# Performance work log

Hardware: AMD Instinct MI355X
Metric: run time of the kernel (lower is better)

The kernel has to match this reference:

```python
import jax, jax.numpy as jnp
import numpy as np

BS, P, D, D_WM, H, W = 64, 512, 1024, 1024, 16, 128
HD = D_WM // H
SCALE = 1.0 / np.sqrt(HD)


def setup_inputs() -> dict:
    key = jax.random.key(0)
    ks = jax.random.split(key, 10)
    s = 0.02
    x_all = jax.random.normal(ks[0], (BS, P, D), dtype=jnp.float32)
    reset_mask_all = jax.random.randint(ks[1], (BS, P), 0, 50) == 0
    return {
        'x_all': x_all,
        'reset_mask_all': reset_mask_all,
        'Wq_w': jax.random.normal(ks[2], (D, D_WM), dtype=jnp.float32) * s,
        'Wq_b': jnp.zeros((D_WM,), jnp.float32),
        'Wk_w': jax.random.normal(ks[3], (D, D_WM), dtype=jnp.float32) * s,
        'Wk_b': jnp.zeros((D_WM,), jnp.float32),
        'Wv_w': jax.random.normal(ks[4], (D, D_WM), dtype=jnp.float32) * s,
        'Wv_b': jnp.zeros((D_WM,), jnp.float32),
        'Wo_w': jax.random.normal(ks[5], (D_WM, D), dtype=jnp.float32) * s,
        'Wo_b': jnp.zeros((D,), jnp.float32),
    }


def _forward_span(x_all, reset_mask_all, Wq_w, Wq_b, Wk_w, Wk_b, Wv_w, Wv_b, Wo_w, Wo_b):
    # Batched projections over all P tokens (matches forward_span)
    q_all = jnp.einsum('bpd,de->bpe', x_all, Wq_w) + Wq_b
    k_all = jnp.einsum('bpd,de->bpe', x_all, Wk_w) + Wk_b
    v_all = jnp.einsum('bpd,de->bpe', x_all, Wv_w) + Wv_b

    def step(carry, inp):
        K, V, valid, ptr = carry  # [BS,W,D_WM], [BS,W,D_WM], [BS,W] bool, [BS] int
        q, k, v, reset_t = inp    # [BS,D_WM] x3, [BS] bool
        # doc-boundary reset
        valid = valid & ~reset_t[:, None]
        ptr = jnp.where(reset_t, 0, ptr)
        # ring-buffer write at ptr (one-hot broadcast, as in the original)
        wm = jnp.arange(W)[None, :] == ptr[:, None]          # [BS,W] bool
        wf = wm.astype(K.dtype)[:, :, None]                   # [BS,W,1]
        K = K * (1.0 - wf) + k[:, None, :] * wf
        V = V * (1.0 - wf) + v[:, None, :] * wf
        valid = valid | wm
        # windowed multi-head attention over the buffer
        qh = q.reshape(BS, H, HD)
        Kh = K.reshape(BS, W, H, HD)
        Vh = V.reshape(BS, W, H, HD)
        attn = jnp.einsum('bhd,bwhd->bhw', qh, Kh) * SCALE
        attn = jnp.where(valid[:, None, :], attn, -jnp.inf)
        attn = jax.nn.softmax(attn, axis=-1)
        attn = jnp.nan_to_num(attn)
        out = jnp.einsum('bhw,bwhd->bhd', attn, Vh).reshape(BS, D_WM)
        y = out @ Wo_w + Wo_b
        ptr = (ptr + 1) % W
        return (K, V, valid, ptr), y

    init = (
        jnp.zeros((BS, W, D_WM), x_all.dtype),
        jnp.zeros((BS, W, D_WM), x_all.dtype),
        jnp.zeros((BS, W), bool),
        jnp.zeros((BS,), jnp.int32),
    )
    xs = (
        q_all.transpose(1, 0, 2),
        k_all.transpose(1, 0, 2),
        v_all.transpose(1, 0, 2),
        reset_mask_all.T,
    )
    _, ys = jax.lax.scan(step, init, xs)  # ys: [P,BS,D]
    return ys.transpose(1, 0, 2)


def reference(x_all, reset_mask_all, Wq_w, Wq_b, Wk_w, Wk_b, Wv_w, Wv_b, Wo_w, Wo_b):
    return _forward_span(x_all, reset_mask_all, Wq_w, Wq_b, Wk_w, Wk_b, Wv_w, Wv_b, Wo_w, Wo_b)
```

## Files before the change

### kernel.cpp

```cpp
#include <hip/hip_runtime.h>
#include <stdint.h>

typedef __bf16 bf16_t;
typedef __bf16 bf16x8 __attribute__((ext_vector_type(8)));
typedef __bf16 bf16x4 __attribute__((ext_vector_type(4)));
typedef float  f32x4  __attribute__((ext_vector_type(4)));

constexpr int cBS = 64, cP = 512, cD = 1024, cDWM = 1024, cH = 16, cHD = 64, cW = 128;
constexpr int cVTP = 672;
constexpr int cM = cBS * cP;
constexpr float cSCALE = 0.125f;

__device__ __forceinline__ void gld_lds16(const void* g, void* l) {
#if __has_builtin(__builtin_amdgcn_global_load_lds)
  __builtin_amdgcn_global_load_lds(
      (__attribute__((address_space(1))) void*)g,
      (__attribute__((address_space(3))) void*)l, 16, 0, 0);
#else
  *(bf16x8*)l = *(const bf16x8*)g;
#endif
}

__global__ void cvt_x_k(const float* __restrict__ X, bf16_t* __restrict__ Y, int n) {
  int i = (blockIdx.x * blockDim.x + threadIdx.x) * 4;
  if (i >= n) return;
  float4 v = *(const float4*)(X + i);
  bf16x4 o;
  o[0] = (bf16_t)v.x; o[1] = (bf16_t)v.y; o[2] = (bf16_t)v.z; o[3] = (bf16_t)v.w;
  *(bf16x4*)(Y + i) = o;
}

__global__ void cvt_wt_k(const float* __restrict__ W0, const float* __restrict__ W1,
                         const float* __restrict__ W2, const float* __restrict__ W3,
                         bf16_t* __restrict__ T0, bf16_t* __restrict__ T1,
                         bf16_t* __restrict__ T2, bf16_t* __restrict__ T3) {
  __shared__ float tile[32][33];
  const float* Wsrc; bf16_t* Tdst;
  switch (blockIdx.z) {
    case 0: Wsrc = W0; Tdst = T0; break;
    case 1: Wsrc = W1; Tdst = T1; break;
    case 2: Wsrc = W2; Tdst = T2; break;
    default: Wsrc = W3; Tdst = T3; break;
  }
  const int n0 = blockIdx.x * 32, k0 = blockIdx.y * 32;
  const int c = threadIdx.x & 31, r8 = threadIdx.x >> 5;
#pragma unroll
  for (int q = 0; q < 4; ++q) {
    int row = r8 + q * 8;
    tile[row][c] = Wsrc[(size_t)(k0 + row) * 1024 + n0 + c];
  }
  __syncthreads();
#pragma unroll
  for (int q = 0; q < 4; ++q) {
    int row = r8 + q * 8;
    Tdst[(size_t)(n0 + row) * 1024 + k0 + c] = (bf16_t)tile[c][row];
  }
}

__global__ void resets2_k(const int* __restrict__ mask, int* __restrict__ r) {
  __shared__ int sm[cP];
  const int b = blockIdx.x, t = threadIdx.x;
  sm[t] = mask[b * cP + t] ? t : 0;
  __syncthreads();
#pragma unroll
  for (int d = 1; d < cP; d <<= 1) {
    int u = (t >= d) ? sm[t - d] : 0;
    __syncthreads();
    if (u > sm[t]) sm[t] = u;
    __syncthreads();
  }
  r[b * cP + t] = sm[t];
}

__global__ __launch_bounds__(512, 2)
void gemm_qkv8_k(const bf16_t* __restrict__ A, const bf16_t* __restrict__ Wt,
                 const float* __restrict__ bq, const float* __restrict__ bk,
                 const float* __restrict__ bvv,
                 bf16_t* __restrict__ Qh, bf16_t* __restrict__ Kh,
                 bf16_t* __restrict__ Vt) {
  __shared__ __align__(16) char LDS[131072];
  const int tid = threadIdx.x;
  const int wid = tid >> 6, ln = tid & 63;
  const int ln15 = ln & 15, g4 = ln >> 4;
  const int wr = wid >> 2, wc = wid & 3;

  const int g = blockIdx.x + 12 * blockIdx.y;
  const int xcd = g & 7, s = g >> 3;
  const int nb = s % 12, mloc = s / 12;
  const int m0 = (xcd * 16 + mloc) * 256, n0 = nb * 256;

  const bf16_t* Ab = A + (size_t)m0 * 1024;
  const bf16_t* Bb = Wt + (size_t)n0 * 1024;

  const int srow = (tid >> 6) * 16 + (tid & 15);
  const int kc = (tid >> 4) & 3;
  const size_t aoff = (size_t)srow * 1024 + (size_t)(kc * 8);
  char* const lbase = LDS + tid * 16;

  const int lane16 = (g4 * 16 + ln15) * 16;
  const int abase = (wr * 8) * 1024 + lane16;
  const int bbase = 32768 + (wc * 4) * 1024 + lane16;

  f32x4 acc[8][4];
#pragma unroll
  for (int i = 0; i < 8; ++i)
#pragma unroll
    for (int j = 0; j < 4; ++j) acc[i][j] = {0.f, 0.f, 0.f, 0.f};

  bf16x8 bq_[4];

#define STAGE_A(buf, kh, j) do {                                              \
    const bf16_t* gp_ = Ab + (size_t)((j) * 64 + (kh) * 32) + aoff;           \
    char* lp_ = lbase + (buf) * 65536 + (kh) * 16384;                         \
    gld_lds16(gp_, lp_);                                                      \
    gld_lds16(gp_ + (size_t)128 * 1024, lp_ + 8192);                          \
  } while (0)

#define STAGE_B(buf, kh, j) do {                                              \
    const bf16_t* gp_ = Bb + (size_t)((j) * 64 + (kh) * 32) + aoff;           \
    char* lp_ = lbase + (buf) * 65536 + (kh) * 16384 + 32768;                 \
    gld_lds16(gp_, lp_);                                                      \
    gld_lds16(gp_ + (size_t)128 * 1024, lp_ + 8192);                          \
  } while (0)

#define NOSTAGE ((void)0)
#define VM4 asm volatile("s_waitcnt vmcnt(4)" ::: "memory")
#define VM0 asm volatile("s_waitcnt vmcnt(0)" ::: "memory")
#define NOVM ((void)0)

#define PHASE_F(buf, kh, STAGE, VME) do {                                     \
    const char* Ar_ = LDS + (buf) * 65536 + (kh) * 16384 + abase;             \
    const char* Br_ = LDS + (buf) * 65536 + (kh) * 16384 + bbase;             \
    bf16x8 af_[4];                                                            \
    af_[0] = *(const bf16x8*)(Ar_);                                           \
    af_[1] = *(const bf16x8*)(Ar_ + 1024);                                    \
    af_[2] = *(const bf16x8*)(Ar_ + 2048);                                    \
    af_[3] = *(const bf16x8*)(Ar_ + 3072);                                    \
    bq_[0] = *(const bf16x8*)(Br_);                                           \
    bq_[1] = *(const bf16x8*)(Br_ + 1024);                                    \
    bq_[2] = *(const bf16x8*)(Br_ + 2048);                                    \
    bq_[3] = *(const bf16x8*)(Br_ + 3072);                                    \
    STAGE;                                                                    \
    __builtin_amdgcn_s_barrier();                                             \
    asm volatile("s_waitcnt lgkmcnt(0)" ::: "memory");                        \
    __builtin_amdgcn_s_setprio(1);                                            \
    _Pragma("unroll")                                                         \
    for (int mi_ = 0; mi_ < 4; ++mi_)                                         \
      _Pragma("unroll")                                                       \
      for (int nj_ = 0; nj_ < 4; ++nj_)                                       \
        acc[mi_][nj_] = __builtin_amdgcn_mfma_f32_16x16x32_bf16(              \
            af_[mi_], bq_[nj_], acc[mi_][nj_], 0, 0, 0);                      \
    __builtin_amdgcn_s_setprio(0);                                            \
    VME;                                                                      \
    __builtin_amdgcn_s_barrier();                                             \
  } while (0)

#define PHASE_R(buf, kh, STAGE, VME) do {                                     \
    const char* Ar_ = LDS + (buf) * 65536 + (kh) * 16384 + abase + 4096;      \
    bf16x8 af_[4];                                                            \
    af_[0] = *(const bf16x8*)(Ar_);                                           \
    af_[1] = *(const bf16x8*)(Ar_ + 1024);                                    \
    af_[2] = *(const bf16x8*)(Ar_ + 2048);                                    \
    af_[3] = *(const bf16x8*)(Ar_ + 3072);                                    \
    STAGE;                                                                    \
    __builtin_amdgcn_s_barrier();                                             \
    asm volatile("s_waitcnt lgkmcnt(0)" ::: "memory");                        \
    __builtin_amdgcn_s_setprio(1);                                            \
    _Pragma("unroll")                                                         \
    for (int mi_ = 0; mi_ < 4; ++mi_)                                         \
      _Pragma("unroll")                                                       \
      for (int nj_ = 0; nj_ < 4; ++nj_)                                       \
        acc[4 + mi_][nj_] = __builtin_amdgcn_mfma_f32_16x16x32_bf16(          \
            af_[mi_], bq_[nj_], acc[4 + mi_][nj_], 0, 0, 0);                  \
    __builtin_amdgcn_s_setprio(0);                                            \
    VME;                                                                      \
    __builtin_amdgcn_s_barrier();                                             \
  } while (0)

  STAGE_A(0, 0, 0); STAGE_B(0, 0, 0); STAGE_A(0, 1, 0); STAGE_B(0, 1, 0);
  asm volatile("s_waitcnt vmcnt(4)" ::: "memory");
  __builtin_amdgcn_s_barrier();

  for (int t = 0; t < 7; ++t) {
    const int j1 = 2 * t + 1, j2 = 2 * t + 2;
    PHASE_F(0, 0, STAGE_A(1, 0, j1), NOVM);
    PHASE_R(0, 0, STAGE_B(1, 0, j1), VM4);
    PHASE_F(0, 1, STAGE_A(1, 1, j1), NOVM);
    PHASE_R(0, 1, STAGE_B(1, 1, j1), VM4);
    PHASE_F(1, 0, STAGE_A(0, 0, j2), NOVM);
    PHASE_R(1, 0, STAGE_B(0, 0, j2), VM4);
    PHASE_F(1, 1, STAGE_A(0, 1, j2), NOVM);
    PHASE_R(1, 1, STAGE_B(0, 1, j2), VM4);
  }
  PHASE_F(0, 0, STAGE_A(1, 0, 15), NOVM);
  PHASE_R(0, 0, STAGE_B(1, 0, 15), VM4);
  PHASE_F(0, 1, STAGE_A(1, 1, 15), NOVM);
  PHASE_R(0, 1, STAGE_B(1, 1, 15), VM4);
  PHASE_F(1, 0, NOSTAGE, NOVM);
  PHASE_R(1, 0, NOSTAGE, VM0);
  PHASE_F(1, 1, NOSTAGE, NOVM);
  PHASE_R(1, 1, NOSTAGE, NOVM);

#undef PHASE_F
#undef PHASE_R
#undef STAGE_A
#undef STAGE_B

  const int seg = n0 >> 10;
  const float* bias = (seg == 0) ? bq : (seg == 1) ? bk : bvv;
  bf16_t* QK = (seg == 0) ? Qh : Kh;
#pragma unroll
  for (int mi = 0; mi < 8; ++mi) {
    const int rbase = m0 + wr * 128 + mi * 16 + g4 * 4;
    const int b = rbase >> 9, pb = rbase & 511;
#pragma unroll
    for (int nj = 0; nj < 4; ++nj) {
      const int col = n0 + wc * 64 + nj * 16 + ln15;
      const int cl = col & 1023;
      const int h = cl >> 6, hd = cl & 63;
      const float bv = bias[cl];
      if (seg < 2) {
#pragma unroll
        for (int r = 0; r < 4; ++r)
          QK[(((size_t)(b * cH + h)) * cP + pb + r) * cHD + hd] =
              (bf16_t)(acc[mi][nj][r] + bv);
      } else {
        bf16x4 pk;
#pragma unroll
        for (int r = 0; r < 4; ++r) pk[r] = (bf16_t)(acc[mi][nj][r] + bv);
        *(bf16x4*)(Vt + ((size_t)((b * cH + h) * cHD + hd)) * cVTP + 128 + pb) = pk;
      }
    }
  }
}

__global__ __launch_bounds__(256)
void gemm_bt_k(const bf16_t* __restrict__ A, const bf16_t* __restrict__ Bt,
               const float* __restrict__ bias, float* __restrict__ C,
               int M, int N, int K) {
  __shared__ __align__(16) bf16_t As[2][128 * 32];
  __shared__ __align__(16) bf16_t Bs[2][128 * 32];
  const int tid = threadIdx.x;
  const int wv = tid >> 6, ln = tid & 63;
  const int ln15 = ln & 15, g4 = ln >> 4;

  const int g = blockIdx.x + 8 * blockIdx.y;
  const int xcd = g & 7, s = g >> 3;
  const int nb = s & 7, mloc = s >> 3;
  const int m0 = (xcd * 32 + mloc) * 128, n0 = nb * 128;

  const int wm = (wv >> 1) * 64, wn = (wv & 1) * 64;
  const bf16_t* Ab = A + (size_t)m0 * K;
  const bf16_t* Bb = Bt + (size_t)n0 * K;

  auto stage = [&](const bf16_t* G, bf16_t* L, int k0) {
#pragma unroll
    for (int gg = 0; gg < 2; ++gg) {
      int slot = gg * 256 + tid;
      gld_lds16(G + (size_t)(slot >> 2) * K + (k0 + (slot & 3) * 8), L + slot * 8);
    }
  };

  f32x4 acc[4][4];
#pragma unroll
  for (int i = 0; i < 4; ++i)
#pragma unroll
    for (int j = 0; j < 4; ++j) acc[i][j] = {0.f, 0.f, 0.f, 0.f};

  const int nk = K >> 5;
  stage(Ab, As[0], 0);
  stage(Bb, Bs[0], 0);
  for (int kt = 0; kt < nk; ++kt) {
    __syncthreads();
    if (kt + 1 < nk) {
      stage(Ab, As[(kt + 1) & 1], (kt + 1) * 32);
      stage(Bb, Bs[(kt + 1) & 1], (kt + 1) * 32);
    }
    const bf16_t* Asb = As[kt & 1];
    const bf16_t* Bsb = Bs[kt & 1];
    bf16x8 af[4], bfr[4];
#pragma unroll
    for (int i = 0; i < 4; ++i)
      af[i] = *(const bf16x8*)(Asb + (wm + i * 16 + ln15) * 32 + g4 * 8);
#pragma unroll
    for (int j = 0; j < 4; ++j)
      bfr[j] = *(const bf16x8*)(Bsb + (wn + j * 16 + ln15) * 32 + g4 * 8);
#pragma unroll
    for (int i = 0; i < 4; ++i)
#pragma unroll
      for (int j = 0; j < 4; ++j)
        acc[i][j] = __builtin_amdgcn_mfma_f32_16x16x32_bf16(af[i], bfr[j], acc[i][j], 0, 0, 0);
  }

#pragma unroll
  for (int i = 0; i < 4; ++i) {
    const int rbase = m0 + wm + i * 16 + g4 * 4;
#pragma unroll
    for (int j = 0; j < 4; ++j) {
      const int col = n0 + wn + j * 16 + ln15;
      const float bv = bias[col];
#pragma unroll
      for (int r = 0; r < 4; ++r)
        C[(size_t)(rbase + r) * N + col] = acc[i][j][r] + bv;
    }
  }
}

__global__ __launch_bounds__(256)
void attn3_k(const bf16_t* __restrict__ Q, const bf16_t* __restrict__ Kv,
             const bf16_t* __restrict__ Vt, const int* __restrict__ rr,
             bf16_t* __restrict__ O) {
  __shared__ __align__(16) bf16_t Pl[4][16][168];
  const int tid = threadIdx.x;
  const int wv = tid >> 6, ln = tid & 63, ln15 = ln & 15, g4 = ln >> 4;
  const int h = blockIdx.x, b = blockIdx.y, tc = blockIdx.z;
  bf16_t(*Pw)[168] = Pl[wv];
  const bf16_t* vb = Vt + ((size_t)(b * cH + h)) * cHD * cVTP;
  const bf16_t* qb = Q + ((size_t)(b * cH + h)) * cP * cHD;
  const bf16_t* kb = Kv + ((size_t)(b * cH + h)) * cP * cHD;

  for (int sub = 0; sub < 2; ++sub) {
    const int t0 = (tc * 2 + sub) * 64 + wv * 16;
    const int sbase = t0 - 128;

    int rv[4];
#pragma unroll
    for (int r = 0; r < 4; ++r) rv[r] = rr[b * cP + t0 + g4 * 4 + r];

    const bf16_t* qp = qb + (size_t)(t0 + ln15) * cHD + g4 * 8;
    const bf16x8 qa0 = *(const bf16x8*)qp;
    const bf16x8 qa1 = *(const bf16x8*)(qp + 32);

    f32x4 lg[9];
#pragma unroll
    for (int c = 0; c < 9; ++c) {
      const int s = sbase + c * 16 + ln15;
      bf16x8 k0v, k1v;
      if ((unsigned)s < (unsigned)cP) {
        const bf16_t* kp = kb + (size_t)s * cHD + g4 * 8;
        k0v = *(const bf16x8*)kp;
        k1v = *(const bf16x8*)(kp + 32);
      } else {
#pragma unroll
        for (int z = 0; z < 8; ++z) { k0v[z] = (bf16_t)0.f; k1v[z] = (bf16_t)0.f; }
      }
      f32x4 a = {0.f, 0.f, 0.f, 0.f};
      a = __builtin_amdgcn_mfma_f32_16x16x32_bf16(qa0, k0v, a, 0, 0, 0);
      a = __builtin_amdgcn_mfma_f32_16x16x32_bf16(qa1, k1v, a, 0, 0, 0);
      lg[c] = a;
    }

    float mx[4] = {-1e30f, -1e30f, -1e30f, -1e30f};
#pragma unroll
    for (int c = 0; c < 9; ++c)
#pragma unroll
      for (int r = 0; r < 4; ++r) {
        const int s = sbase + c * 16 + ln15;
        const int t = t0 + g4 * 4 + r;
        const bool ok = (s >= rv[r]) && (s <= t) && (t - s < cW);
        const float l = ok ? lg[c][r] * cSCALE : -1e30f;
        lg[c][r] = l;
        mx[r] = fmaxf(mx[r], l);
      }
#pragma unroll
    for (int r = 0; r < 4; ++r) {
      mx[r] = fmaxf(mx[r], __shfl_xor(mx[r], 1));
      mx[r] = fmaxf(mx[r], __shfl_xor(mx[r], 2));
      mx[r] = fmaxf(mx[r], __shfl_xor(mx[r], 4));
      mx[r] = fmaxf(mx[r], __shfl_xor(mx[r], 8));
    }
    float sm[4] = {0.f, 0.f, 0.f, 0.f};
#pragma unroll
    for (int c = 0; c < 9; ++c)
#pragma unroll
      for (int r = 0; r < 4; ++r) {
        const float e = __expf(lg[c][r] - mx[r]);
        lg[c][r] = e;
        sm[r] += e;
      }
#pragma unroll
    for (int r = 0; r < 4; ++r) {
      sm[r] += __shfl_xor(sm[r], 1);
      sm[r] += __shfl_xor(sm[r], 2);
      sm[r] += __shfl_xor(sm[r], 4);
      sm[r] += __shfl_xor(sm[r], 8);
    }
    float inv[4];
#pragma unroll
    for (int r = 0; r < 4; ++r) inv[r] = 1.f / sm[r];

#pragma unroll
    for (int c = 0; c < 9; ++c)
#pragma unroll
      for (int r = 0; r < 4; ++r)
        Pw[g4 * 4 + r][c * 16 + ln15] = (bf16_t)(lg[c][r] * inv[r]);
#pragma unroll
    for (int z = 0; z < 4; ++z)
      Pw[ln15][144 + g4 * 4 + z] = (bf16_t)0.f;

    f32x4 oacc[4];
#pragma unroll
    for (int j = 0; j < 4; ++j) oacc[j] = {0.f, 0.f, 0.f, 0.f};
#pragma unroll
    for (int c2 = 0; c2 < 5; ++c2) {
      const bf16x8 pa = *(const bf16x8*)(&Pw[ln15][c2 * 32 + g4 * 8]);
#pragma unroll
      for (int j = 0; j < 4; ++j) {
        const bf16x8 vf =
            *(const bf16x8*)(vb + (size_t)(j * 16 + ln15) * cVTP + (t0 + c2 * 32 + g4 * 8));
        oacc[j] = __builtin_amdgcn_mfma_f32_16x16x32_bf16(pa, vf, oacc[j], 0, 0, 0);
      }
    }
#pragma unroll
    for (int j = 0; j < 4; ++j) {
      const int col = h * cHD + j * 16 + ln15;
#pragma unroll
      for (int r = 0; r < 4; ++r)
        O[((size_t)(b * cP + t0 + g4 * 4 + r)) * cDWM + col] = (bf16_t)oacc[j][r];
    }
  }
}

extern "C" void kernel_launch(void* const* d_in, const int* in_sizes, int n_in,
                              void* d_out, int out_size, void* d_ws, size_t ws_size,
                              hipStream_t stream) {
  (void)in_sizes; (void)n_in; (void)out_size; (void)ws_size;
  const float* x  = (const float*)d_in[0];
  const int* mask = (const int*)d_in[1];
  const float* Wq = (const float*)d_in[2];
  const float* bq = (const float*)d_in[3];
  const float* Wk = (const float*)d_in[4];
  const float* bk = (const float*)d_in[5];
  const float* Wv = (const float*)d_in[6];
  const float* bv = (const float*)d_in[7];
  const float* Wo = (const float*)d_in[8];
  const float* bo = (const float*)d_in[9];
  float* out = (float*)d_out;

  char* ws = (char*)d_ws;
  size_t off = 0;
  bf16_t* Xbf = (bf16_t*)(ws + off); off += (size_t)cM * cD * 2;
  bf16_t* Wqt = (bf16_t*)(ws + off); off += (size_t)cD * cDWM * 2;
  bf16_t* Wkt = (bf16_t*)(ws + off); off += (size_t)cD * cDWM * 2;
  bf16_t* Wvt = (bf16_t*)(ws + off); off += (size_t)cD * cDWM * 2;
  bf16_t* Wot = (bf16_t*)(ws + off); off += (size_t)cDWM * cD * 2;
  bf16_t* Qh  = (bf16_t*)(ws + off); off += (size_t)cM * cDWM * 2;
  bf16_t* Kh  = (bf16_t*)(ws + off); off += (size_t)cM * cDWM * 2;
  bf16_t* Vt  = (bf16_t*)(ws + off); off += (size_t)cBS * cH * cHD * cVTP * 2;
  int* rbuf   = (int*)(ws + off);    off += (size_t)cBS * cP * 4;
  bf16_t* Ob  = Xbf;

  cvt_x_k<<<(cM * cD / 4 + 255) / 256, 256, 0, stream>>>(x, Xbf, cM * cD);
  cvt_wt_k<<<dim3(32, 32, 4), 256, 0, stream>>>(Wq, Wk, Wv, Wo, Wqt, Wkt, Wvt, Wot);
  resets2_k<<<cBS, cP, 0, stream>>>(mask, rbuf);

  gemm_qkv8_k<<<dim3(12, 128), 512, 0, stream>>>(Xbf, Wqt, bq, bk, bv, Qh, Kh, Vt);

  attn3_k<<<dim3(cH, cBS, 4), 256, 0, stream>>>(Qh, Kh, Vt, rbuf, Ob);

  gemm_bt_k<<<dim3(8, 256), 256, 0, stream>>>(Ob, Wot, bo, out, cM, cD, cDWM);
}
```

Baseline: 546.8 us.

## Stage GEMM tiles through registers instead of direct global-to-LDS loads

Replaces the global_load_lds direct-to-LDS staging in the QKV projection GEMM with a register-staged pipeline. Each phase writes the previously loaded tile to LDS and issues global loads for a future tile into registers, with one lgkmcnt wait plus barrier per phase instead of two barriers. The aim is to hide global latency behind the MFMA work and cut synchronisation. In exchange it uses more VGPRs and adds LDS write instructions, and the implicit vmcnt waits the compiler inserts before the LDS stores could stall.

```diff
diff --git a/kernel.cpp b/kernel.cpp
--- a/kernel.cpp
+++ b/kernel.cpp
@@ -5,6 +5,7 @@
 typedef __bf16 bf16x8 __attribute__((ext_vector_type(8)));
 typedef __bf16 bf16x4 __attribute__((ext_vector_type(4)));
 typedef float  f32x4  __attribute__((ext_vector_type(4)));
+typedef uint32_t u32x4 __attribute__((ext_vector_type(4)));
 
 constexpr int cBS = 64, cP = 512, cD = 1024, cDWM = 1024, cH = 16, cHD = 64, cW = 128;
 constexpr int cVTP = 672;
@@ -95,11 +96,10 @@
   const int srow = (tid >> 6) * 16 + (tid & 15);
   const int kc = (tid >> 4) & 3;
   const size_t aoff = (size_t)srow * 1024 + (size_t)(kc * 8);
-  char* const lbase = LDS + tid * 16;
 
   const int lane16 = (g4 * 16 + ln15) * 16;
   const int abase = (wr * 8) * 1024 + lane16;
-  const int bbase = 32768 + (wc * 4) * 1024 + lane16;
+  const int bbase = (wc * 4) * 1024 + lane16;
 
   f32x4 acc[8][4];
 #pragma unroll
@@ -107,104 +107,105 @@
 #pragma unroll
     for (int j = 0; j < 4; ++j) acc[i][j] = {0.f, 0.f, 0.f, 0.f};
 
-  bf16x8 bq_[4];
-
-#define STAGE_A(buf, kh, j) do {                                              \
-    const bf16_t* gp_ = Ab + (size_t)((j) * 64 + (kh) * 32) + aoff;           \
-    char* lp_ = lbase + (buf) * 65536 + (kh) * 16384;                         \
-    gld_lds16(gp_, lp_);                                                      \
-    gld_lds16(gp_ + (size_t)128 * 1024, lp_ + 8192);                          \
+  bf16x8 bqf[4];
+  u32x4 p0a, p0b, p1a, p1b;
+
+#define GLOADP(p, BASE, j, kh) do {                                           \
+    const bf16_t* g_ = (BASE) + (size_t)((j) * 64 + (kh) * 32) + aoff;        \
+    p##a = *(const u32x4*)g_;                                                 \
+    p##b = *(const u32x4*)(g_ + (size_t)128 * 1024);                          \
   } while (0)
 
-#define STAGE_B(buf, kh, j) do {                                              \
-    const bf16_t* gp_ = Bb + (size_t)((j) * 64 + (kh) * 32) + aoff;           \
-    char* lp_ = lbase + (buf) * 65536 + (kh) * 16384 + 32768;                 \
-    gld_lds16(gp_, lp_);                                                      \
-    gld_lds16(gp_ + (size_t)128 * 1024, lp_ + 8192);                          \
+#define LDSW(p, buf, kh, isB) do {                                            \
+    char* w_ = LDS + (buf) * 65536 + (kh) * 16384 + (isB) * 32768 + tid * 16; \
+    *(u32x4*)w_ = p##a;                                                       \
+    *(u32x4*)(w_ + 8192) = p##b;                                              \
   } while (0)
 
-#define NOSTAGE ((void)0)
-#define VM4 asm volatile("s_waitcnt vmcnt(4)" ::: "memory")
-#define VM0 asm volatile("s_waitcnt vmcnt(0)" ::: "memory")
-#define NOVM ((void)0)
-
-#define PHASE_F(buf, kh, STAGE, VME) do {                                     \
+#define FENCE asm volatile("s_waitcnt lgkmcnt(0)\ns_barrier" ::: "memory")
+#define NOP ((void)0)
+
+#define PHASE_F(buf, kh, WR, ISS) do {                                        \
+    WR;                                                                       \
+    ISS;                                                                      \
     const char* Ar_ = LDS + (buf) * 65536 + (kh) * 16384 + abase;             \
-    const char* Br_ = LDS + (buf) * 65536 + (kh) * 16384 + bbase;             \
+    const char* Br_ = LDS + (buf) * 65536 + (kh) * 16384 + 32768 + bbase;     \
     bf16x8 af_[4];                                                            \
     af_[0] = *(const bf16x8*)(Ar_);                                           \
     af_[1] = *(const bf16x8*)(Ar_ + 1024);                                    \
     af_[2] = *(const bf16x8*)(Ar_ + 2048);                                    \
     af_[3] = *(const bf16x8*)(Ar_ + 3072);                                    \
-    bq_[0] = *(const bf16x8*)(Br_);                                           \
-    bq_[1] = *(const bf16x8*)(Br_ + 1024);                                    \
-    bq_[2] = *(const bf16x8*)(Br_ + 2048);                                    \
-    bq_[3] = *(const bf16x8*)(Br_ + 3072);                                    \
-    STAGE;                                                                    \
-    __builtin_amdgcn_s_barrier();                                             \
-    asm volatile("s_waitcnt lgkmcnt(0)" ::: "memory");                        \
+    bqf[0] = *(const bf16x8*)(Br_);                                           \
+    bqf[1] = *(const bf16x8*)(Br_ + 1024);                                    \
+    bqf[2] = *(const bf16x8*)(Br_ + 2048);                                    \
+    bqf[3] = *(const bf16x8*)(Br_ + 3072);                                    \
     __builtin_amdgcn_s_setprio(1);                                            \
     _Pragma("unroll")                                                         \
     for (int mi_ = 0; mi_ < 4; ++mi_)                                         \
       _Pragma("unroll")                                                       \
       for (int nj_ = 0; nj_ < 4; ++nj_)                                       \
         acc[mi_][nj_] = __builtin_amdgcn_mfma_f32_16x16x32_bf16(              \
-            af_[mi_], bq_[nj_], acc[mi_][nj_], 0, 0, 0);                      \
+            af_[mi_], bqf[nj_], acc[mi_][nj_], 0, 0, 0);                      \
     __builtin_amdgcn_s_setprio(0);                                            \
-    VME;                                                                      \
-    __builtin_amdgcn_s_barrier();                                             \
+    FENCE;                                                                    \
   } while (0)
 
-#define PHASE_R(buf, kh, STAGE, VME) do {                                     \
+#define PHASE_R(buf, kh, WR, ISS) do {                                        \
+    WR;                                                                       \
+    ISS;                                                                      \
     const char* Ar_ = LDS + (buf) * 65536 + (kh) * 16384 + abase + 4096;      \
     bf16x8 af_[4];                                                            \
     af_[0] = *(const bf16x8*)(Ar_);                                           \
     af_[1] = *(const bf16x8*)(Ar_ + 1024);                                    \
     af_[2] = *(const bf16x8*)(Ar_ + 2048);                                    \
     af_[3] = *(const bf16x8*)(Ar_ + 3072);                                    \
-    STAGE;                                                                    \
-    __builtin_amdgcn_s_barrier();                                             \
-    asm volatile("s_waitcnt lgkmcnt(0)" ::: "memory");                        \
     __builtin_amdgcn_s_setprio(1);                                            \
     _Pragma("unroll")                                                         \
     for (int mi_ = 0; mi_ < 4; ++mi_)                                         \
       _Pragma("unroll")                                                       \
       for (int nj_ = 0; nj_ < 4; ++nj_)                                       \
         acc[4 + mi_][nj_] = __builtin_amdgcn_mfma_f32_16x16x32_bf16(          \
-            af_[mi_], bq_[nj_], acc[4 + mi_][nj_], 0, 0, 0);                  \
+            af_[mi_], bqf[nj_], acc[4 + mi_][nj_], 0, 0, 0);                  \
     __builtin_amdgcn_s_setprio(0);                                            \
-    VME;                                                                      \
-    __builtin_amdgcn_s_barrier();                                             \
+    FENCE;                                                                    \
   } while (0)
 
-  STAGE_A(0, 0, 0); STAGE_B(0, 0, 0); STAGE_A(0, 1, 0); STAGE_B(0, 1, 0);
-  asm volatile("s_waitcnt vmcnt(4)" ::: "memory");
-  __builtin_amdgcn_s_barrier();
+  {
+    u32x4 q0a, q0b, q1a, q1b;
+    GLOADP(p0, Ab, 0, 0); GLOADP(p1, Bb, 0, 0);
+    GLOADP(q0, Ab, 0, 1); GLOADP(q1, Bb, 0, 1);
+    LDSW(p0, 0, 0, 0); LDSW(p1, 0, 0, 1);
+    LDSW(q0, 0, 1, 0); LDSW(q1, 0, 1, 1);
+    GLOADP(p0, Ab, 1, 0); GLOADP(p1, Bb, 1, 0);
+    FENCE;
+  }
 
   for (int t = 0; t < 7; ++t) {
-    const int j1 = 2 * t + 1, j2 = 2 * t + 2;
-    PHASE_F(0, 0, STAGE_A(1, 0, j1), NOVM);
-    PHASE_R(0, 0, STAGE_B(1, 0, j1), VM4);
-    PHASE_F(0, 1, STAGE_A(1, 1, j1), NOVM);
-    PHASE_R(0, 1, STAGE_B(1, 1, j1), VM4);
-    PHASE_F(1, 0, STAGE_A(0, 0, j2), NOVM);
-    PHASE_R(1, 0, STAGE_B(0, 0, j2), VM4);
-    PHASE_F(1, 1, STAGE_A(0, 1, j2), NOVM);
-    PHASE_R(1, 1, STAGE_B(0, 1, j2), VM4);
-  }
-  PHASE_F(0, 0, STAGE_A(1, 0, 15), NOVM);
-  PHASE_R(0, 0, STAGE_B(1, 0, 15), VM4);
-  PHASE_F(0, 1, STAGE_A(1, 1, 15), NOVM);
-  PHASE_R(0, 1, STAGE_B(1, 1, 15), VM4);
-  PHASE_F(1, 0, NOSTAGE, NOVM);
-  PHASE_R(1, 0, NOSTAGE, VM0);
-  PHASE_F(1, 1, NOSTAGE, NOVM);
-  PHASE_R(1, 1, NOSTAGE, NOVM);
+    const int j1 = 2 * t + 1, j2 = 2 * t + 2, j3 = 2 * t + 3;
+    PHASE_F(0, 0, LDSW(p0, 1, 0, 0), GLOADP(p0, Ab, j1, 1));
+    PHASE_R(0, 0, LDSW(p1, 1, 0, 1), GLOADP(p1, Bb, j1, 1));
+    PHASE_F(0, 1, LDSW(p0, 1, 1, 0), GLOADP(p0, Ab, j2, 0));
+    PHASE_R(0, 1, LDSW(p1, 1, 1, 1), GLOADP(p1, Bb, j2, 0));
+    PHASE_F(1, 0, LDSW(p0, 0, 0, 0), GLOADP(p0, Ab, j2, 1));
+    PHASE_R(1, 0, LDSW(p1, 0, 0, 1), GLOADP(p1, Bb, j2, 1));
+    PHASE_F(1, 1, LDSW(p0, 0, 1, 0), GLOADP(p0, Ab, j3, 0));
+    PHASE_R(1, 1, LDSW(p1, 0, 1, 1), GLOADP(p1, Bb, j3, 0));
+  }
+  PHASE_F(0, 0, LDSW(p0, 1, 0, 0), GLOADP(p0, Ab, 15, 1));
+  PHASE_R(0, 0, LDSW(p1, 1, 0, 1), GLOADP(p1, Bb, 15, 1));
+  PHASE_F(0, 1, LDSW(p0, 1, 1, 0), NOP);
+  PHASE_R(0, 1, LDSW(p1, 1, 1, 1), NOP);
+  PHASE_F(1, 0, NOP, NOP);
+  PHASE_R(1, 0, NOP, NOP);
+  PHASE_F(1, 1, NOP, NOP);
+  PHASE_R(1, 1, NOP, NOP);
 
 #undef PHASE_F
 #undef PHASE_R
-#undef STAGE_A
-#undef STAGE_B
+#undef GLOADP
+#undef LDSW
+#undef FENCE
+#undef NOP
 
   const int seg = n0 >> 10;
   const float* bias = (seg == 0) ? bq : (seg == 1) ? bk : bvv;
```

After: 953.0 us. 74.3% more time.
